# Performance work log

Measured on AMD Instinct MI355X. Metric: run time of the kernel, lower is better.

Reference implementation:

```python
import jax, jax.numpy as jnp
import numpy as np

N = 50000      # nodes
E = 800000     # edges (avg degree 16)
H = 128        # hidden_nf
NORM_FACTOR = 100.0   # normalization_factor, aggregation 'sum'
NORM_CONST = 1.0      # norm_constant (effective_constant = max(1, 1.0))
EPS = 1e-8


def silu(v):
    return v * jax.nn.sigmoid(v)


def setup_inputs() -> dict:
    key = jax.random.key(0)
    ks = jax.random.split(key, 16)
    IN_E = 2 * H + 2  # edge MLP input: h[row] | h[col] | [radial, edge_attr]

    def w(k, shape, scale=0.05):
        return jax.random.normal(k, shape, dtype=jnp.float32) * scale

    return {
        "h": jax.random.normal(ks[0], (N, H), dtype=jnp.float32),
        "x": jax.random.normal(ks[1], (N, 3), dtype=jnp.float32),
        "edge_index": jax.random.randint(ks[2], (2, E), 0, N, dtype=jnp.int32),
        "edge_attr": jax.random.normal(ks[3], (E, 1), dtype=jnp.float32),
        "node_mask": jnp.ones((N, 1), dtype=jnp.float32),
        "edge_mask": jnp.ones((E, 1), dtype=jnp.float32),
        # 2 stacked GCL layers (identical shapes -> stacked on leading dim)
        "gcl_e_w1": w(ks[4], (2, IN_E, H)), "gcl_e_b1": jnp.zeros((2, H), jnp.float32),
        "gcl_e_w2": w(ks[5], (2, H, H)),    "gcl_e_b2": jnp.zeros((2, H), jnp.float32),
        "gcl_a_w":  w(ks[6], (2, H, 1)),    "gcl_a_b":  jnp.zeros((2, 1), jnp.float32),
        "gcl_n_w1": w(ks[7], (2, 2 * H, H)),"gcl_n_b1": jnp.zeros((2, H), jnp.float32),
        "gcl_n_w2": w(ks[8], (2, H, H)),    "gcl_n_b2": jnp.zeros((2, H), jnp.float32),
        # EquivariantUpdate coord MLP (last layer xavier gain 0.001 -> tiny, no bias)
        "c_w1": w(ks[9], (IN_E, H)), "c_b1": jnp.zeros((H,), jnp.float32),
        "c_w2": w(ks[10], (H, H)),   "c_b2": jnp.zeros((H,), jnp.float32),
        "c_w3": w(ks[11], (H, 1), 0.001),
    }


def reference(h, x, edge_index, edge_attr, node_mask, edge_mask,
              gcl_e_w1, gcl_e_b1, gcl_e_w2, gcl_e_b2, gcl_a_w, gcl_a_b,
              gcl_n_w1, gcl_n_b1, gcl_n_w2, gcl_n_b2,
              c_w1, c_b1, c_w2, c_b2, c_w3):
    row, col = edge_index[0], edge_index[1]
    n_nodes = h.shape[0]

    # coord2diff
    diff = x[row] - x[col]                                  # [E,3]
    radial = jnp.sum(diff * diff, axis=1, keepdims=True)    # [E,1]
    norm = jnp.sqrt(radial + EPS)
    coord_diff = diff / (norm + NORM_CONST)

    # edge_attr = cat([distances, edge_attr])  -> edge_feat_nf = 2
    ea = jnp.concatenate([radial, edge_attr], axis=1)       # [E,2]

    # n_layers=2 GCLs with attention
    for i in range(2):
        einp = jnp.concatenate([h[row], h[col], ea], axis=1)             # [E,258]
        mij = silu(silu(einp @ gcl_e_w1[i] + gcl_e_b1[i]) @ gcl_e_w2[i] + gcl_e_b2[i])
        att = jax.nn.sigmoid(mij @ gcl_a_w[i] + gcl_a_b[i])
        ef = mij * att * edge_mask                                       # [E,H]
        agg = jax.ops.segment_sum(ef, row, num_segments=n_nodes) / NORM_FACTOR
        ninp = jnp.concatenate([h, agg], axis=1)                         # [N,2H]
        h = h + (silu(ninp @ gcl_n_w1[i] + gcl_n_b1[i]) @ gcl_n_w2[i] + gcl_n_b2[i])
        h = h * node_mask

    # EquivariantUpdate (tanh=False, reflection_equiv=True -> no cross term)
    einp = jnp.concatenate([h[row], h[col], ea], axis=1)
    phi = silu(silu(einp @ c_w1 + c_b1) @ c_w2 + c_b2) @ c_w3            # [E,1]
    trans = coord_diff * phi * edge_mask                                 # [E,3]
    aggx = jax.ops.segment_sum(trans, row, num_segments=n_nodes) / NORM_FACTOR
    x = (x + aggx) * node_mask

    h = h * node_mask
    return (h, x)
```

## Files before the change

kernel.cpp:

```cpp
#include <hip/hip_runtime.h>
#include <hip/hip_bf16.h>
#include <math.h>
#include <string.h>

#define DEV __device__ __forceinline__

typedef __bf16 bf16;
typedef bf16 bf16x8 __attribute__((ext_vector_type(8)));
typedef bf16 bf16x2 __attribute__((ext_vector_type(2)));
typedef float f32x4 __attribute__((ext_vector_type(4)));
typedef unsigned int uint;

constexpr int N_NODES = 50000;
constexpr int N_EDGES = 800000;
constexpr int H = 128;
constexpr int NB_SCAN = (N_NODES + 255) / 256;

DEV float fsilu(float x) { return x / (1.f + __expf(-x)); }
DEV float fsigmoid(float x) { return 1.f / (1.f + __expf(-x)); }


__global__ void transpose_pad_kernel(bf16* __restrict__ dst, const float* __restrict__ src,
                                     int K, int Nf, int KP) {
    int idx = blockIdx.x * 256 + threadIdx.x;
    if (idx >= Nf * KP) return;
    int n = idx / KP, k = idx - n * KP;
    dst[idx] = (k < K) ? (bf16)src[k * Nf + n] : (bf16)0.f;
}

__global__ void h_init_kernel(const float* __restrict__ h, float* __restrict__ h_cur, int n) {
    int i = blockIdx.x * 256 + threadIdx.x;
    if (i < n) h_cur[i] = h[i];
}

__global__ void out_h_kernel(const float* __restrict__ h_cur, const float* __restrict__ nmask,
                             float* __restrict__ out) {
    int i = blockIdx.x * 256 + threadIdx.x;
    if (i < N_NODES * H) out[i] = h_cur[i] * nmask[i >> 7];
}


__global__ void count_kernel(const int* __restrict__ ei, int* __restrict__ deg) {
    int e = blockIdx.x * 256 + threadIdx.x;
    if (e < N_EDGES) atomicAdd(&deg[ei[e]], 1);
}

__global__ void scan1_kernel(const int* __restrict__ deg, int* __restrict__ off,
                             int* __restrict__ bsum) {
    __shared__ int s[256];
    int t = threadIdx.x, i = blockIdx.x * 256 + t;
    int v = (i < N_NODES) ? deg[i] : 0;
    s[t] = v;
    __syncthreads();
#pragma unroll
    for (int st = 1; st < 256; st <<= 1) {
        int x = (t >= st) ? s[t - st] : 0;
        __syncthreads();
        s[t] += x;
        __syncthreads();
    }
    if (i < N_NODES) off[i] = s[t] - v;
    if (t == 255) bsum[blockIdx.x] = s[255];
}

__global__ void scan2_kernel(int* __restrict__ bsum) {
    __shared__ int s[256];
    int t = threadIdx.x;
    int v = (t < NB_SCAN) ? bsum[t] : 0;
    s[t] = v;
    __syncthreads();
#pragma unroll
    for (int st = 1; st < 256; st <<= 1) {
        int x = (t >= st) ? s[t - st] : 0;
        __syncthreads();
        s[t] += x;
        __syncthreads();
    }
    if (t < NB_SCAN) bsum[t] = s[t] - v;
}

__global__ void scan3_kernel(int* __restrict__ off, const int* __restrict__ bsum) {
    int i = blockIdx.x * 256 + threadIdx.x;
    if (i >= N_NODES) return;
    off[i] += bsum[blockIdx.x];
}

__global__ void fill2_kernel(const int* __restrict__ ei, const float* __restrict__ eattr,
                             const float* __restrict__ emask, int* __restrict__ off,
                             uint* __restrict__ rc_pm, bf16* __restrict__ eaem_pm) {
    int e = blockIdx.x * 256 + threadIdx.x;
    if (e >= N_EDGES) return;
    int r = ei[e], c = ei[N_EDGES + e];
    int slot = atomicAdd(&off[r], 1);
    rc_pm[slot] = ((uint)r << 16) | (uint)c;
    eaem_pm[(size_t)slot * 2 + 0] = (bf16)eattr[e];
    eaem_pm[(size_t)slot * 2 + 1] = (bf16)emask[e];
}

__global__ __launch_bounds__(256, 2) void pq_kernel(
    const float* __restrict__ h_cur, const bf16* __restrict__ w1t,
    const float* __restrict__ b1, bf16* __restrict__ P, bf16* __restrict__ Q) {
    __shared__ __align__(16) bf16 hs[64 * 128];
    int t = threadIdx.x, lane = t & 63, wv = t >> 6;
    int lr = lane & 15, lg = lane >> 4;
    int nbase = blockIdx.x * 64;

    {
        int nl = t >> 2, q = t & 3;
        int node = nbase + nl;
        if (node < N_NODES) {
            const float4* hr = (const float4*)(h_cur + (size_t)node * H);
#pragma unroll
            for (int c = 0; c < 4; ++c) {
                float4 v0 = hr[q * 8 + c * 2];
                float4 v1 = hr[q * 8 + c * 2 + 1];
                bf16x8 o;
                o[0] = (bf16)v0.x; o[1] = (bf16)v0.y; o[2] = (bf16)v0.z; o[3] = (bf16)v0.w;
                o[4] = (bf16)v1.x; o[5] = (bf16)v1.y; o[6] = (bf16)v1.z; o[7] = (bf16)v1.w;
                int sl = (q * 4 + c) ^ (nl & 7);
                *(bf16x8*)(hs + nl * 128 + sl * 8) = o;
            }
        } else {
#pragma unroll
            for (int c = 0; c < 4; ++c) {
                int sl = (q * 4 + c) ^ (nl & 7);
                *(bf16x8*)(hs + nl * 128 + sl * 8) = (bf16x8)(bf16)0.f;
            }
        }
    }
    __syncthreads();

    f32x4 aP[4][2], aQ[4][2];
#pragma unroll
    for (int er = 0; er < 4; ++er)
#pragma unroll
        for (int j = 0; j < 2; ++j) { aP[er][j] = (f32x4)0.f; aQ[er][j] = (f32x4)0.f; }

    const bf16* bp0 = w1t + (size_t)((wv * 2 + 0) * 16 + lr) * 256 + lg * 8;
    const bf16* bp1 = w1t + (size_t)((wv * 2 + 1) * 16 + lr) * 256 + lg * 8;
#pragma unroll
    for (int kk = 0; kk < 4; ++kk) {
        bf16x8 a[4];
#pragma unroll
        for (int er = 0; er < 4; ++er) {
            int sl = (kk * 4 + lg) ^ (lr & 7);
            a[er] = *(const bf16x8*)(hs + (er * 16 + lr) * 128 + sl * 8);
        }
        bf16x8 bP0 = *(const bf16x8*)(bp0 + kk * 32);
        bf16x8 bP1 = *(const bf16x8*)(bp1 + kk * 32);
        bf16x8 bQ0 = *(const bf16x8*)(bp0 + 128 + kk * 32);
        bf16x8 bQ1 = *(const bf16x8*)(bp1 + 128 + kk * 32);
#pragma unroll
        for (int er = 0; er < 4; ++er) {
            aP[er][0] = __builtin_amdgcn_mfma_f32_16x16x32_bf16(a[er], bP0, aP[er][0], 0, 0, 0);
            aP[er][1] = __builtin_amdgcn_mfma_f32_16x16x32_bf16(a[er], bP1, aP[er][1], 0, 0, 0);
            aQ[er][0] = __builtin_amdgcn_mfma_f32_16x16x32_bf16(a[er], bQ0, aQ[er][0], 0, 0, 0);
            aQ[er][1] = __builtin_amdgcn_mfma_f32_16x16x32_bf16(a[er], bQ1, aQ[er][1], 0, 0, 0);
        }
    }

    float bb0 = b1[(wv * 2 + 0) * 16 + lr];
    float bb1v = b1[(wv * 2 + 1) * 16 + lr];
#pragma unroll
    for (int er = 0; er < 4; ++er) {
#pragma unroll
        for (int j = 0; j < 2; ++j) {
            int feat = (wv * 2 + j) * 16 + lr;
            float bb = j ? bb1v : bb0;
#pragma unroll
            for (int r = 0; r < 4; ++r) {
                int node = nbase + er * 16 + lg * 4 + r;
                if (node < N_NODES) {
                    P[(size_t)node * H + feat] = (bf16)(aP[er][j][r] + bb);
                    Q[(size_t)node * H + feat] = (bf16)(aQ[er][j][r]);
                }
            }
        }
    }
}


__global__ __launch_bounds__(256) void gather_h_kernel(
    const bf16* __restrict__ ef, const int* __restrict__ off, bf16* __restrict__ agg_bf) {
    int t = threadIdx.x, lane = t & 63, wv = t >> 6;
    int n = blockIdx.x * 4 + wv;
    if (n >= N_NODES) return;
    int st = (n == 0) ? 0 : off[n - 1];
    int dg = off[n] - st;
    const bf16* bp = ef + (size_t)st * H + lane * 2;
    float s0 = 0.f, s1 = 0.f;
    for (int k = 0; k < dg; ++k) {
        uint v = *(const uint*)(bp + (size_t)k * H);
        s0 += __uint_as_float(v << 16);
        s1 += __uint_as_float(v & 0xffff0000u);
    }
    bf16x2 o;
    o[0] = (bf16)(s0 * 0.01f);
    o[1] = (bf16)(s1 * 0.01f);
    *(bf16x2*)(agg_bf + (size_t)n * H + lane * 2) = o;
}

__global__ __launch_bounds__(256) void gather_x_kernel(
    const float* __restrict__ trans, const int* __restrict__ off,
    const float* __restrict__ x, const float* __restrict__ nmask, float* __restrict__ outx) {
    int t = threadIdx.x, lane = t & 63, wv = t >> 6;
    int n = blockIdx.x * 4 + wv;
    if (n >= N_NODES) return;
    int st = (n == 0) ? 0 : off[n - 1];
    int dg = off[n] - st;
    float sx = 0.f, sy = 0.f, sz = 0.f;
    for (int k = lane; k < dg; k += 64) {
        const float* tp = trans + (size_t)(st + k) * 3;
        sx += tp[0];
        sy += tp[1];
        sz += tp[2];
    }
#pragma unroll
    for (int m = 1; m < 64; m <<= 1) {
        sx += __shfl_xor(sx, m);
        sy += __shfl_xor(sy, m);
        sz += __shfl_xor(sz, m);
    }
    if (lane == 0) {
        float nm = nmask[n];
        outx[n * 3 + 0] = (x[n * 3 + 0] + sx * 0.01f) * nm;
        outx[n * 3 + 1] = (x[n * 3 + 1] + sy * 0.01f) * nm;
        outx[n * 3 + 2] = (x[n * 3 + 2] + sz * 0.01f) * nm;
    }
}


template <int KCHUNKS, int ASTRIDE, int BSTRIDE>
DEV void wave_gemm(const bf16* A_lds, const bf16* __restrict__ Bt,
                   f32x4 (&acc)[4][2], int lr, int lg, int wv) {
#pragma unroll
    for (int kk = 0; kk < KCHUNKS; ++kk) {
        int ko = kk * 32 + lg * 8;
        bf16x8 a[4], b[2];
#pragma unroll
        for (int er = 0; er < 4; ++er)
            a[er] = *(const bf16x8*)(A_lds + (er * 16 + lr) * ASTRIDE + ko);
#pragma unroll
        for (int j = 0; j < 2; ++j)
            b[j] = *(const bf16x8*)(Bt + (size_t)((wv * 2 + j) * 16 + lr) * BSTRIDE + ko);
#pragma unroll
        for (int er = 0; er < 4; ++er)
#pragma unroll
            for (int j = 0; j < 2; ++j)
                acc[er][j] = __builtin_amdgcn_mfma_f32_16x16x32_bf16(a[er], b[j], acc[er][j], 0, 0, 0);
    }
}

DEV void epi_silu_store(const f32x4 (&acc)[4][2], const float* __restrict__ bias,
                        bf16* out_lds, int OSTRIDE, int lr, int lg, int wv) {
    float b0 = bias[(wv * 2 + 0) * 16 + lr];
    float b1 = bias[(wv * 2 + 1) * 16 + lr];
#pragma unroll
    for (int er = 0; er < 4; ++er) {
#pragma unroll
        for (int j = 0; j < 2; ++j) {
            float bb = j ? b1 : b0;
            int fcol = (wv * 2 + j) * 16 + lr;
#pragma unroll
            for (int r = 0; r < 4; ++r) {
                int rrow = er * 16 + lg * 4 + r;
                out_lds[rrow * OSTRIDE + fcol] = (bf16)fsilu(acc[er][j][r] + bb);
            }
        }
    }
}

DEV void epi_silu_store_swz(const f32x4 (&acc)[4][2], const float* __restrict__ bias,
                            bf16* out_lds, int lr, int lg, int wv) {
    float b0 = bias[(wv * 2 + 0) * 16 + lr];
    float b1 = bias[(wv * 2 + 1) * 16 + lr];
#pragma unroll
    for (int er = 0; er < 4; ++er) {
#pragma unroll
        for (int j = 0; j < 2; ++j) {
            float bb = j ? b1 : b0;
            int fcol = (wv * 2 + j) * 16 + lr;
#pragma unroll
            for (int r = 0; r < 4; ++r) {
                int rrow = er * 16 + lg * 4 + r;
                int sl = (fcol >> 3) ^ (rrow & 7);
                out_lds[rrow * 128 + sl * 8 + (fcol & 7)] = (bf16)fsilu(acc[er][j][r] + bb);
            }
        }
    }
}

template <int MODE>
__global__ __launch_bounds__(256, 8) void edge_kernel(
    const bf16* __restrict__ P, const bf16* __restrict__ Q,
    const uint* __restrict__ rc_pm, const bf16* __restrict__ eaem_pm,
    const float* __restrict__ xg,
    const float* __restrict__ w_r, const float* __restrict__ w_e,
    const bf16* __restrict__ w2t, const float* __restrict__ b2,
    const float* __restrict__ avec, const float* __restrict__ abias,
    bf16* __restrict__ efout, float* __restrict__ trans) {
    __shared__ __align__(16) bf16 T[64 * 128];
    __shared__ __align__(16) float avec_l[128];
    __shared__ __align__(16) float wr_l[128];
    __shared__ __align__(16) float we_l[128];

    int t = threadIdx.x, lane = t & 63, wv = t >> 6;
    int lr = lane & 15, lg = lane >> 4;
    int ebase = blockIdx.x * 64;
    int el = t >> 2, q = t & 3;

    {
        int rsub = lane >> 4;
        int slot = lane & 15;
#pragma unroll
        for (int u = 0; u < 4; ++u) {
            int r = wv * 16 + u * 4 + rsub;
            uint rcs = rc_pm[ebase + r];
            int nc = (int)(rcs & 0xffffu);
            int sl = slot ^ (r & 7);
            const bf16* gpc = Q + (size_t)nc * H + sl * 8;
            __builtin_amdgcn_global_load_lds(
                (const __attribute__((address_space(1))) void*)gpc,
                (__attribute__((address_space(3))) void*)&T[(wv * 16 + u * 4) * 128],
                16, 0, 0);
        }
    }
    if (t < 128) {
        avec_l[t] = avec[t];
    } else {
        wr_l[t - 128] = w_r[t - 128];
        we_l[t - 128] = w_e[t - 128];
    }

    uint rc = rc_pm[ebase + el];
    int rr = (int)(rc >> 16), cc = (int)(rc & 0xffffu);
    float dx = xg[rr * 3 + 0] - xg[cc * 3 + 0];
    float dy = xg[rr * 3 + 1] - xg[cc * 3 + 1];
    float dz = xg[rr * 3 + 2] - xg[cc * 3 + 2];
    float radial = dx * dx + dy * dy + dz * dz;
    uint eu = *(const uint*)(eaem_pm + (size_t)(ebase + el) * 2);
    bf16x2 ep = __builtin_bit_cast(bf16x2, eu);
    float eattr = (float)ep[0];
    float em = (float)ep[1];

    bf16x8 pvr[4];
    const bf16* Pp = P + (size_t)rr * H + q * 32;
#pragma unroll
    for (int c = 0; c < 4; ++c) pvr[c] = *(const bf16x8*)(Pp + c * 8);

    __syncthreads();

#pragma unroll
    for (int c = 0; c < 4; ++c) {
        int sl = (q * 4 + c) ^ (el & 7);
        bf16* ap = T + el * 128 + sl * 8;
        bf16x8 qv = *(const bf16x8*)ap;
        bf16x8 pv = pvr[c];
        f32x4 wr0 = *(const f32x4*)(wr_l + q * 32 + c * 8);
        f32x4 wr1 = *(const f32x4*)(wr_l + q * 32 + c * 8 + 4);
        f32x4 we0 = *(const f32x4*)(we_l + q * 32 + c * 8);
        f32x4 we1 = *(const f32x4*)(we_l + q * 32 + c * 8 + 4);
        bf16x8 o;
#pragma unroll
        for (int jj = 0; jj < 4; ++jj) {
            float v = (float)pv[jj] + (float)qv[jj] + radial * wr0[jj] + eattr * we0[jj];
            o[jj] = (bf16)fsilu(v);
        }
#pragma unroll
        for (int jj = 0; jj < 4; ++jj) {
            float v = (float)pv[4 + jj] + (float)qv[4 + jj] + radial * wr1[jj] + eattr * we1[jj];
            o[4 + jj] = (bf16)fsilu(v);
        }
        *(bf16x8*)ap = o;
    }
    __syncthreads();

    f32x4 acc2[4][2];
#pragma unroll
    for (int er = 0; er < 4; ++er)
#pragma unroll
        for (int j = 0; j < 2; ++j) acc2[er][j] = (f32x4)0.f;
    {
        const bf16* cp0 = w2t + (size_t)((wv * 2 + 0) * 16 + lr) * 128 + lg * 8;
        const bf16* cp1 = w2t + (size_t)((wv * 2 + 1) * 16 + lr) * 128 + lg * 8;
#pragma unroll
        for (int kk = 0; kk < 4; ++kk) {
            bf16x8 a[4], b[2];
            b[0] = *(const bf16x8*)(cp0 + kk * 32);
            b[1] = *(const bf16x8*)(cp1 + kk * 32);
#pragma unroll
            for (int er = 0; er < 4; ++er) {
                int sl = (kk * 4 + lg) ^ (lr & 7);
                a[er] = *(const bf16x8*)(T + (er * 16 + lr) * 128 + sl * 8);
            }
#pragma unroll
            for (int er = 0; er < 4; ++er)
#pragma unroll
                for (int j = 0; j < 2; ++j)
                    acc2[er][j] = __builtin_amdgcn_mfma_f32_16x16x32_bf16(a[er], b[j], acc2[er][j], 0, 0, 0);
        }
    }
    __syncthreads();

    epi_silu_store_swz(acc2, b2, T, lr, lg, wv);
    __syncthreads();

    float part = 0.f;
    bf16x8 mv[4];
#pragma unroll
    for (int c = 0; c < 4; ++c) {
        int sl = (q * 4 + c) ^ (el & 7);
        mv[c] = *(const bf16x8*)(T + el * 128 + sl * 8);
        f32x4 av0 = *(const f32x4*)(avec_l + q * 32 + c * 8);
        f32x4 av1 = *(const f32x4*)(avec_l + q * 32 + c * 8 + 4);
#pragma unroll
        for (int jj = 0; jj < 4; ++jj) part += (float)mv[c][jj] * av0[jj];
#pragma unroll
        for (int jj = 0; jj < 4; ++jj) part += (float)mv[c][4 + jj] * av1[jj];
    }
    part += __shfl_xor(part, 1);
    part += __shfl_xor(part, 2);

    if (MODE == 0) {
        float att = fsigmoid(part + abias[0]);
        float scale = att * em;
        bf16* edst = efout + (size_t)(ebase + el) * H + q * 32;
#pragma unroll
        for (int c = 0; c < 4; ++c) {
            bf16x8 o;
#pragma unroll
            for (int jj = 0; jj < 8; ++jj) o[jj] = (bf16)((float)mv[c][jj] * scale);
            *(bf16x8*)(edst + c * 8) = o;
        }
    } else {
        if (q == 0) {
            float inv = 1.f / (sqrtf(radial + 1e-8f) + 1.f);
            float s = part * em * inv;
            int sI = ebase + el;
            trans[sI * 3 + 0] = dx * s;
            trans[sI * 3 + 1] = dy * s;
            trans[sI * 3 + 2] = dz * s;
        }
    }
}

__global__ __launch_bounds__(256, 2) void node_kernel(
    float* __restrict__ h_cur, const bf16* __restrict__ agg_bf,
    const bf16* __restrict__ w1t, const float* __restrict__ b1,
    const bf16* __restrict__ w2t, const float* __restrict__ b2,
    const float* __restrict__ nmask) {
    constexpr int SRN = 264;
    constexpr int TRN = 136;
    __shared__ __align__(16) bf16 ninp[64 * SRN];
    __shared__ __align__(16) bf16 t1[64 * TRN];

    int t = threadIdx.x, lane = t & 63, wv = t >> 6;
    int lr = lane & 15, lg = lane >> 4;
    int nbase = blockIdx.x * 64;

    {
        int nl = t >> 2, q = t & 3;
        int node = nbase + nl;
        bf16* dst = ninp + nl * SRN;
        if (node < N_NODES) {
            const float4* hr = (const float4*)(h_cur + (size_t)node * H);
            const bf16* ar = agg_bf + (size_t)node * H;
#pragma unroll
            for (int pp = 0; pp < 8; ++pp) {
                int ch = pp * 4 + q;
                float4 v = hr[ch];
                dst[ch * 4 + 0] = (bf16)v.x; dst[ch * 4 + 1] = (bf16)v.y;
                dst[ch * 4 + 2] = (bf16)v.z; dst[ch * 4 + 3] = (bf16)v.w;
            }
#pragma unroll
            for (int pp = 0; pp < 4; ++pp) {
                int ch = pp * 4 + q;
                *(bf16x8*)(dst + 128 + ch * 8) = *(const bf16x8*)(ar + ch * 8);
            }
        } else {
#pragma unroll
            for (int pp = 0; pp < 8; ++pp) {
                int ch = pp * 4 + q;
#pragma unroll
                for (int k = 0; k < 4; ++k) {
                    dst[ch * 4 + k] = (bf16)0.f;
                    dst[128 + ch * 4 + k] = (bf16)0.f;
                }
            }
        }
    }
    __syncthreads();

    f32x4 acc[4][2];
#pragma unroll
    for (int er = 0; er < 4; ++er)
#pragma unroll
        for (int j = 0; j < 2; ++j) acc[er][j] = (f32x4)0.f;
    wave_gemm<8, SRN, 256>(ninp, w1t, acc, lr, lg, wv);
    epi_silu_store(acc, b1, t1, TRN, lr, lg, wv);
    __syncthreads();

    f32x4 acc2[4][2];
#pragma unroll
    for (int er = 0; er < 4; ++er)
#pragma unroll
        for (int j = 0; j < 2; ++j) acc2[er][j] = (f32x4)0.f;
    wave_gemm<4, TRN, 128>(t1, w2t, acc2, lr, lg, wv);

    float bb0 = b2[(wv * 2 + 0) * 16 + lr];
    float bb1 = b2[(wv * 2 + 1) * 16 + lr];
#pragma unroll
    for (int er = 0; er < 4; ++er) {
#pragma unroll
        for (int j = 0; j < 2; ++j) {
            float bb = j ? bb1 : bb0;
            int feat = (wv * 2 + j) * 16 + lr;
#pragma unroll
            for (int r = 0; r < 4; ++r) {
                int node = nbase + er * 16 + lg * 4 + r;
                if (node < N_NODES) {
                    size_t idx = (size_t)node * H + feat;
                    float nm = nmask[node];
                    h_cur[idx] = (h_cur[idx] + acc2[er][j][r] + bb) * nm;
                }
            }
        }
    }
}

extern "C" void kernel_launch(void* const* d_in, const int* in_sizes, int n_in,
                              void* d_out, int out_size, void* d_ws, size_t ws_size,
                              hipStream_t stream) {
    (void)in_sizes; (void)n_in; (void)out_size; (void)ws_size;
    const float* h_in  = (const float*)d_in[0];
    const float* x_in  = (const float*)d_in[1];
    const int*   ei    = (const int*)d_in[2];
    const float* eattr = (const float*)d_in[3];
    const float* nmask = (const float*)d_in[4];
    const float* emask = (const float*)d_in[5];
    const float* e_w1  = (const float*)d_in[6];
    const float* e_b1  = (const float*)d_in[7];
    const float* e_w2  = (const float*)d_in[8];
    const float* e_b2  = (const float*)d_in[9];
    const float* a_w   = (const float*)d_in[10];
    const float* a_b   = (const float*)d_in[11];
    const float* n_w1  = (const float*)d_in[12];
    const float* n_b1  = (const float*)d_in[13];
    const float* n_w2  = (const float*)d_in[14];
    const float* n_b2  = (const float*)d_in[15];
    const float* c_w1  = (const float*)d_in[16];
    const float* c_b1  = (const float*)d_in[17];
    const float* c_w2  = (const float*)d_in[18];
    const float* c_b2  = (const float*)d_in[19];
    const float* c_w3  = (const float*)d_in[20];
    float* out = (float*)d_out;

    char* p = (char*)d_ws;
    auto alloc = [&](size_t bytes) { char* r = p; p += (bytes + 255) & ~(size_t)255; return r; };
    float* h_cur  = (float*)alloc((size_t)N_NODES * H * 4);
    bf16*  Pb     = (bf16*) alloc((size_t)N_NODES * H * 2);
    bf16*  Qb     = (bf16*) alloc((size_t)N_NODES * H * 2);
    bf16*  agg_bf = Qb;
    bf16*  ef     = (bf16*) alloc((size_t)N_EDGES * H * 2);
    float* trans  = (float*)ef;
    int*   deg    = (int*)  alloc((size_t)N_NODES * 4);
    int*   off    = (int*)  alloc((size_t)N_NODES * 4);
    int*   bsum   = (int*)  alloc((size_t)NB_SCAN * 4);
    uint*  rc_pm  = (uint*) alloc((size_t)N_EDGES * 4);
    bf16*  eaem_pm= (bf16*) alloc((size_t)N_EDGES * 2 * 2);
    bf16*  e_w1t  = (bf16*) alloc((size_t)2 * 128 * 256 * 2);
    bf16*  e_w2t  = (bf16*) alloc((size_t)2 * 128 * 128 * 2);
    bf16*  n_w1t  = (bf16*) alloc((size_t)2 * 128 * 256 * 2);
    bf16*  n_w2t  = (bf16*) alloc((size_t)2 * 128 * 128 * 2);
    bf16*  c_w1t  = (bf16*) alloc((size_t)128 * 256 * 2);
    bf16*  c_w2t  = (bf16*) alloc((size_t)128 * 128 * 2);

    auto tp = [&](bf16* dst, const float* src, int K, int KP) {
        int tot = 128 * KP;
        transpose_pad_kernel<<<(tot + 255) / 256, 256, 0, stream>>>(dst, src, K, 128, KP);
    };
    tp(e_w1t, e_w1, 258, 256);               tp(e_w1t + 128 * 256, e_w1 + 258 * 128, 258, 256);
    tp(e_w2t, e_w2, 128, 128);               tp(e_w2t + 128 * 128, e_w2 + 128 * 128, 128, 128);
    tp(n_w1t, n_w1, 256, 256);               tp(n_w1t + 128 * 256, n_w1 + 256 * 128, 256, 256);
    tp(n_w2t, n_w2, 128, 128);               tp(n_w2t + 128 * 128, n_w2 + 128 * 128, 128, 128);
    tp(c_w1t, c_w1, 258, 256);
    tp(c_w2t, c_w2, 128, 128);

    h_init_kernel<<<(N_NODES * H + 255) / 256, 256, 0, stream>>>(h_in, h_cur, N_NODES * H);

    hipMemsetAsync(deg, 0, (size_t)N_NODES * 4, stream);
    count_kernel<<<(N_EDGES + 255) / 256, 256, 0, stream>>>(ei, deg);
    scan1_kernel<<<NB_SCAN, 256, 0, stream>>>(deg, off, bsum);
    scan2_kernel<<<1, 256, 0, stream>>>(bsum);
    scan3_kernel<<<NB_SCAN, 256, 0, stream>>>(off, bsum);
    fill2_kernel<<<(N_EDGES + 255) / 256, 256, 0, stream>>>(
        ei, eattr, emask, off, rc_pm, eaem_pm);

    int ngrid = (N_NODES + 3) / 4;
    int pqgrid = (N_NODES + 63) / 64;
    for (int i = 0; i < 2; ++i) {
        pq_kernel<<<pqgrid, 256, 0, stream>>>(
            h_cur, e_w1t + (size_t)i * 128 * 256, e_b1 + i * H, Pb, Qb);
        edge_kernel<0><<<N_EDGES / 64, 256, 0, stream>>>(
            Pb, Qb, rc_pm, eaem_pm, x_in,
            e_w1 + (size_t)i * 258 * 128 + 256 * 128,
            e_w1 + (size_t)i * 258 * 128 + 257 * 128,
            e_w2t + (size_t)i * 128 * 128, e_b2 + i * H,
            a_w + i * H, a_b + i, ef, nullptr);
        gather_h_kernel<<<ngrid, 256, 0, stream>>>(ef, off, agg_bf);
        node_kernel<<<(N_NODES + 63) / 64, 256, 0, stream>>>(
            h_cur, agg_bf,
            n_w1t + (size_t)i * 128 * 256, n_b1 + i * H,
            n_w2t + (size_t)i * 128 * 128, n_b2 + i * H, nmask);
    }
    pq_kernel<<<pqgrid, 256, 0, stream>>>(h_cur, c_w1t, c_b1, Pb, Qb);
    edge_kernel<1><<<N_EDGES / 64, 256, 0, stream>>>(
        Pb, Qb, rc_pm, eaem_pm, x_in,
        c_w1 + 256 * 128, c_w1 + 257 * 128,
        c_w2t, c_b2, c_w3, nullptr, nullptr, trans);
    gather_x_kernel<<<ngrid, 256, 0, stream>>>(trans, off, x_in, nmask,
                                               out + (size_t)N_NODES * H);

    out_h_kernel<<<(N_NODES * H + 255) / 256, 256, 0, stream>>>(h_cur, nmask, out);
}
```

Baseline: 881.2 us.

## Store edge messages as fp8 and compute attention dot with MFMA

The per-edge message buffer written by the edge kernel and read by the node gather is now stored as fp8 (e4m3) instead of bf16. This halves the dominant E×H write and read traffic. The attention logit dot product is moved from a per-thread scalar loop with shuffles onto an MFMA using a single-column B operand, with results passed through a small shared array. The first-layer elementwise math is rewritten with packed float2 operations. The trade-off is a real precision loss on aggregated messages, which may risk tolerance, plus an extra block synchronisation.

```diff
diff --git a/kernel.cpp b/kernel.cpp
--- a/kernel.cpp
+++ b/kernel.cpp
@@ -9,7 +9,10 @@
 typedef bf16 bf16x8 __attribute__((ext_vector_type(8)));
 typedef bf16 bf16x2 __attribute__((ext_vector_type(2)));
 typedef float f32x4 __attribute__((ext_vector_type(4)));
+typedef float f32x2 __attribute__((ext_vector_type(2)));
 typedef unsigned int uint;
+typedef unsigned char uchar;
+typedef unsigned short ushort;
 
 constexpr int N_NODES = 50000;
 constexpr int N_EDGES = 800000;
@@ -181,18 +184,19 @@
 
 
 __global__ __launch_bounds__(256) void gather_h_kernel(
-    const bf16* __restrict__ ef, const int* __restrict__ off, bf16* __restrict__ agg_bf) {
+    const uchar* __restrict__ ef, const int* __restrict__ off, bf16* __restrict__ agg_bf) {
     int t = threadIdx.x, lane = t & 63, wv = t >> 6;
     int n = blockIdx.x * 4 + wv;
     if (n >= N_NODES) return;
     int st = (n == 0) ? 0 : off[n - 1];
     int dg = off[n] - st;
-    const bf16* bp = ef + (size_t)st * H + lane * 2;
+    const uchar* bp = ef + (size_t)st * 128 + lane * 2;
     float s0 = 0.f, s1 = 0.f;
     for (int k = 0; k < dg; ++k) {
-        uint v = *(const uint*)(bp + (size_t)k * H);
-        s0 += __uint_as_float(v << 16);
-        s1 += __uint_as_float(v & 0xffff0000u);
+        uint v = *(const ushort*)(bp + (size_t)k * 128);
+        f32x2 f = __builtin_amdgcn_cvt_pk_f32_fp8(v, false);
+        s0 += f.x;
+        s1 += f.y;
     }
     bf16x2 o;
     o[0] = (bf16)(s0 * 0.01f);
@@ -298,11 +302,11 @@
     const float* __restrict__ w_r, const float* __restrict__ w_e,
     const bf16* __restrict__ w2t, const float* __restrict__ b2,
     const float* __restrict__ avec, const float* __restrict__ abias,
-    bf16* __restrict__ efout, float* __restrict__ trans) {
+    uchar* __restrict__ efout, float* __restrict__ trans) {
     __shared__ __align__(16) bf16 T[64 * 128];
-    __shared__ __align__(16) float avec_l[128];
     __shared__ __align__(16) float wr_l[128];
     __shared__ __align__(16) float we_l[128];
+    __shared__ float part_l[64];
 
     int t = threadIdx.x, lane = t & 63, wv = t >> 6;
     int lr = lane & 15, lg = lane >> 4;
@@ -326,9 +330,8 @@
         }
     }
     if (t < 128) {
-        avec_l[t] = avec[t];
+        wr_l[t] = w_r[t];
     } else {
-        wr_l[t - 128] = w_r[t - 128];
         we_l[t - 128] = w_e[t - 128];
     }
 
@@ -350,26 +353,25 @@
 
     __syncthreads();
 
+    f32x2 rad2 = {radial, radial};
+    f32x2 ea2 = {eattr, eattr};
 #pragma unroll
     for (int c = 0; c < 4; ++c) {
         int sl = (q * 4 + c) ^ (el & 7);
         bf16* ap = T + el * 128 + sl * 8;
-        bf16x8 qv = *(const bf16x8*)ap;
-        bf16x8 pv = pvr[c];
-        f32x4 wr0 = *(const f32x4*)(wr_l + q * 32 + c * 8);
-        f32x4 wr1 = *(const f32x4*)(wr_l + q * 32 + c * 8 + 4);
-        f32x4 we0 = *(const f32x4*)(we_l + q * 32 + c * 8);
-        f32x4 we1 = *(const f32x4*)(we_l + q * 32 + c * 8 + 4);
+        uint4 qu = __builtin_bit_cast(uint4, *(const bf16x8*)ap);
+        uint4 pu = __builtin_bit_cast(uint4, pvr[c]);
         bf16x8 o;
 #pragma unroll
-        for (int jj = 0; jj < 4; ++jj) {
-            float v = (float)pv[jj] + (float)qv[jj] + radial * wr0[jj] + eattr * we0[jj];
-            o[jj] = (bf16)fsilu(v);
-        }
-#pragma unroll
-        for (int jj = 0; jj < 4; ++jj) {
-            float v = (float)pv[4 + jj] + (float)qv[4 + jj] + radial * wr1[jj] + eattr * we1[jj];
-            o[4 + jj] = (bf16)fsilu(v);
+        for (int k = 0; k < 4; ++k) {
+            uint puk = (&pu.x)[k], quk = (&qu.x)[k];
+            f32x2 p2 = {__uint_as_float(puk << 16), __uint_as_float(puk & 0xffff0000u)};
+            f32x2 q2 = {__uint_as_float(quk << 16), __uint_as_float(quk & 0xffff0000u)};
+            f32x2 w2 = *(const f32x2*)(wr_l + q * 32 + c * 8 + k * 2);
+            f32x2 e2 = *(const f32x2*)(we_l + q * 32 + c * 8 + k * 2);
+            f32x2 v = p2 + q2 + rad2 * w2 + ea2 * e2;
+            o[2 * k + 0] = (bf16)fsilu(v.x);
+            o[2 * k + 1] = (bf16)fsilu(v.y);
         }
         *(bf16x8*)ap = o;
     }
@@ -405,32 +407,60 @@
     epi_silu_store_swz(acc2, b2, T, lr, lg, wv);
     __syncthreads();
 
-    float part = 0.f;
-    bf16x8 mv[4];
-#pragma unroll
-    for (int c = 0; c < 4; ++c) {
-        int sl = (q * 4 + c) ^ (el & 7);
-        mv[c] = *(const bf16x8*)(T + el * 128 + sl * 8);
-        f32x4 av0 = *(const f32x4*)(avec_l + q * 32 + c * 8);
-        f32x4 av1 = *(const f32x4*)(avec_l + q * 32 + c * 8 + 4);
-#pragma unroll
-        for (int jj = 0; jj < 4; ++jj) part += (float)mv[c][jj] * av0[jj];
-#pragma unroll
-        for (int jj = 0; jj < 4; ++jj) part += (float)mv[c][4 + jj] * av1[jj];
-    }
-    part += __shfl_xor(part, 1);
-    part += __shfl_xor(part, 2);
+    {
+        f32x4 dacc = (f32x4)0.f;
+#pragma unroll
+        for (int kk = 0; kk < 4; ++kk) {
+            int sl = (kk * 4 + lg) ^ (lr & 7);
+            bf16x8 a = *(const bf16x8*)(T + (wv * 16 + lr) * 128 + sl * 8);
+            bf16x8 b = (bf16x8)(bf16)0.f;
+            if (lr == 0) {
+#pragma unroll
+                for (int i = 0; i < 8; ++i) b[i] = (bf16)avec[kk * 32 + lg * 8 + i];
+            }
+            dacc = __builtin_amdgcn_mfma_f32_16x16x32_bf16(a, b, dacc, 0, 0, 0);
+        }
+        if (lr == 0) {
+#pragma unroll
+            for (int r = 0; r < 4; ++r) part_l[wv * 16 + lg * 4 + r] = dacc[r];
+        }
+    }
+    __syncthreads();
+
+    float part = part_l[el];
 
     if (MODE == 0) {
         float att = fsigmoid(part + abias[0]);
         float scale = att * em;
-        bf16* edst = efout + (size_t)(ebase + el) * H + q * 32;
-#pragma unroll
-        for (int c = 0; c < 4; ++c) {
-            bf16x8 o;
-#pragma unroll
-            for (int jj = 0; jj < 8; ++jj) o[jj] = (bf16)((float)mv[c][jj] * scale);
-            *(bf16x8*)(edst + c * 8) = o;
+        f32x2 sc2 = {scale, scale};
+        uchar* edst = efout + (size_t)(ebase + el) * 128 + q * 32;
+#pragma unroll
+        for (int cpair = 0; cpair < 2; ++cpair) {
+            uint4 wout;
+#pragma unroll
+            for (int cc = 0; cc < 2; ++cc) {
+                int c = cpair * 2 + cc;
+                int sl = (q * 4 + c) ^ (el & 7);
+                uint4 mu = __builtin_bit_cast(uint4, *(const bf16x8*)(T + el * 128 + sl * 8));
+                uint w0 = 0, w1 = 0;
+                {
+                    uint m0 = (&mu.x)[0], m1 = (&mu.x)[1];
+                    f32x2 a2 = f32x2{__uint_as_float(m0 << 16), __uint_as_float(m0 & 0xffff0000u)} * sc2;
+                    f32x2 b2v = f32x2{__uint_as_float(m1 << 16), __uint_as_float(m1 & 0xffff0000u)} * sc2;
+                    w0 = __builtin_amdgcn_cvt_pk_fp8_f32(a2.x, a2.y, w0, false);
+                    w0 = __builtin_amdgcn_cvt_pk_fp8_f32(b2v.x, b2v.y, w0, true);
+                }
+                {
+                    uint m2 = (&mu.x)[2], m3 = (&mu.x)[3];
+                    f32x2 a2 = f32x2{__uint_as_float(m2 << 16), __uint_as_float(m2 & 0xffff0000u)} * sc2;
+                    f32x2 b2v = f32x2{__uint_as_float(m3 << 16), __uint_as_float(m3 & 0xffff0000u)} * sc2;
+                    w1 = __builtin_amdgcn_cvt_pk_fp8_f32(a2.x, a2.y, w1, false);
+                    w1 = __builtin_amdgcn_cvt_pk_fp8_f32(b2v.x, b2v.y, w1, true);
+                }
+                (&wout.x)[cc * 2 + 0] = w0;
+                (&wout.x)[cc * 2 + 1] = w1;
+            }
+            *(uint4*)(edst + cpair * 16) = wout;
         }
     } else {
         if (q == 0) {
@@ -561,7 +591,7 @@
     bf16*  Pb     = (bf16*) alloc((size_t)N_NODES * H * 2);
     bf16*  Qb     = (bf16*) alloc((size_t)N_NODES * H * 2);
     bf16*  agg_bf = Qb;
-    bf16*  ef     = (bf16*) alloc((size_t)N_EDGES * H * 2);
+    uchar* ef     = (uchar*)alloc((size_t)N_EDGES * 128);
     float* trans  = (float*)ef;
     int*   deg    = (int*)  alloc((size_t)N_NODES * 4);
     int*   off    = (int*)  alloc((size_t)N_NODES * 4);
```

Result: faster. 807.0 us, median of 2 (-8.4%).
